# Performance work log

Hardware: AMD Instinct MI355X
Metric: run time of the kernel (lower is better)

The kernel has to match this reference:

```python
import jax, jax.numpy as jnp
import numpy as np

K = 10          # number of clusters (static; matches randint fill_max)
ALPHA = 0.02    # intra-cluster margin
DELTA = 0.5     # inter-cluster margin
LAMBDA_INTRA = 1.0
LAMBDA_INTER = 1.0
MIN_WEIGHT = 50.0


def setup_inputs() -> dict:
    key = jax.random.key(0)
    k1, k2 = jax.random.split(key)
    x = jax.random.normal(k1, (8, 64, 240, 320), dtype=jnp.float32)
    # module assumes NORMALIZED unit vectors along channel dim
    x = x / jnp.maximum(jnp.linalg.norm(x, axis=1, keepdims=True), 1e-12)
    cluster_masks = jax.random.randint(k2, (8, 1, 240, 320), 0, K, dtype=jnp.int32)
    return {"x": x, "cluster_masks": cluster_masks}


def reference(x, cluster_masks):
    B, C, H, W = x.shape
    cm = cluster_masks[:, 0]  # (B, H, W) int
    # one-hot cluster assignment; out-of-range ids (e.g. -1 = unlabeled) -> all zeros
    onehot = jax.nn.one_hot(cm, K, dtype=x.dtype)  # (B, H, W, K)

    # ---- spherical cluster means (fused segment-reduce over H*W) ----
    sums = jnp.einsum('bchw,bhwk->bck', x, onehot)          # (B, C, K)
    counts = jnp.sum(onehot, axis=(1, 2))                    # (B, K)
    means = sums / (counts[:, None, :] + 1e-10)
    # F.normalize(p=2, dim=1): x / max(||x||, eps)
    means = means / jnp.maximum(jnp.linalg.norm(means, axis=1, keepdims=True), 1e-12)

    # ---- broadcast means back to pixels ----
    tiled = jnp.einsum('bck,bhwk->bchw', means, onehot)      # (B, C, H, W)

    labeled = (cm >= 0).astype(x.dtype)                      # (B, H, W)
    # cosine metric
    intra_d = labeled * (0.5 * (1.0 - jnp.sum(x * tiled, axis=1)))  # (B, H, W)

    # ---- per-cluster hard-example weighting ----
    indicator = (intra_d > ALPHA).astype(x.dtype)            # (B, H, W)
    N_k = jnp.einsum('bhw,bhwk->bk', indicator, onehot)      # (B, K)
    weights = jnp.einsum('bk,bhwk->bhw', N_k, onehot)        # (B, H, W)
    weights = jnp.maximum(weights, MIN_WEIGHT) * K
    intra_loss = jnp.sum(intra_d ** 2 / weights) / B
    intra_loss = LAMBDA_INTRA * jnp.where(jnp.sum(indicator) > 0, intra_loss, 0.0)

    # ---- inter-cluster hinge loss (K > 1 statically) ----
    inter_d = 0.5 * (1.0 - jnp.einsum('bck,bcl->bkl', means, means))  # (B, K, K)
    hinge = jnp.maximum(DELTA - inter_d, 0.0) * (1.0 - jnp.eye(K, dtype=x.dtype))
    inter_loss = LAMBDA_INTER * jnp.sum(hinge ** 2) / (K * (K - 1) / 2 * B)

    loss = intra_loss + inter_loss
    return (loss, intra_loss, inter_loss)
```

## Files before the change

### kernel.cpp

```cpp
#include <hip/hip_runtime.h>

#define B_ 8
#define C_ 64
#define H_ 240
#define W_ 320
#define HW_ (H_ * W_)
#define HW4_ (HW_ / 4)
#define K_ 10
#define ALPHA_ 0.02f
#define DELTA_ 0.5f
#define MIN_WEIGHT_ 50.0f

#define NCH 4
#define CB_ (C_ / NCH)
#define Z1 8


__global__ __launch_bounds__(256) void k1_sums(
    const float* __restrict__ x, const int* __restrict__ cm,
    float* __restrict__ sums, float* __restrict__ counts) {
  const int cb = blockIdx.x;
  const int b = blockIdx.y;
  const int z = blockIdx.z;
  const int tid = threadIdx.x;
  const int c0 = cb * NCH;

  const int chunk = HW4_ / Z1;
  const int lo = z * chunk;
  const int hi = lo + chunk;

  const float4* __restrict__ xp =
      (const float4*)(x + (size_t)(b * C_ + c0) * HW_);
  const int4* __restrict__ cp = (const int4*)(cm + (size_t)b * HW_);

  float acc[NCH][K_];
#pragma unroll
  for (int c = 0; c < NCH; ++c)
#pragma unroll
    for (int j = 0; j < K_; ++j) acc[c][j] = 0.f;

  float cnt[K_];
#pragma unroll
  for (int j = 0; j < K_; ++j) cnt[j] = 0.f;
  const bool do_cnt = (cb == 0);

  for (int i = lo + tid; i < hi; i += 256) {
    const int4 k4 = cp[i];

    float oh0[K_], oh1[K_], oh2[K_], oh3[K_];
#pragma unroll
    for (int j = 0; j < K_; ++j) {
      oh0[j] = (k4.x == j) ? 1.f : 0.f;
      oh1[j] = (k4.y == j) ? 1.f : 0.f;
      oh2[j] = (k4.z == j) ? 1.f : 0.f;
      oh3[j] = (k4.w == j) ? 1.f : 0.f;
    }
    if (do_cnt) {
#pragma unroll
      for (int j = 0; j < K_; ++j)
        cnt[j] += (oh0[j] + oh1[j]) + (oh2[j] + oh3[j]);
    }

#pragma unroll
    for (int c = 0; c < NCH; ++c) {
      const float4 v = xp[c * HW4_ + i];
#pragma unroll
      for (int j = 0; j < K_; ++j) {
        acc[c][j] += v.x * oh0[j];
        acc[c][j] += v.y * oh1[j];
        acc[c][j] += v.z * oh2[j];
        acc[c][j] += v.w * oh3[j];
      }
    }
  }

#pragma unroll
  for (int c = 0; c < NCH; ++c) {
#pragma unroll
    for (int j = 0; j < K_; ++j) {
      float v = acc[c][j];
#pragma unroll
      for (int off = 32; off > 0; off >>= 1) v += __shfl_down(v, off, 64);
      if ((tid & 63) == 0)
        atomicAdd(&sums[(b * C_ + c0 + c) * K_ + j], v);
    }
  }
  if (do_cnt) {
#pragma unroll
    for (int j = 0; j < K_; ++j) {
      float v = cnt[j];
#pragma unroll
      for (int off = 32; off > 0; off >>= 1) v += __shfl_down(v, off, 64);
      if ((tid & 63) == 0) atomicAdd(&counts[b * K_ + j], v);
    }
  }
}

__global__ __launch_bounds__(256) void k3_intra(
    const float* __restrict__ x, const int* __restrict__ cm,
    const float* __restrict__ sums, const float* __restrict__ counts,
    float* __restrict__ means, float* __restrict__ S2,
    float* __restrict__ Nk) {
  const int b = blockIdx.y;
  const int chunk = blockIdx.x;
  const int tid = threadIdx.x;
  const int lane_p = tid & 63;
  const int grp = tid >> 6;

  __shared__ float mlds[C_ * K_];
  __shared__ float nrm[K_];
  __shared__ float4 pd[256];
  __shared__ float s2b[K_];
  __shared__ float nkb[K_];

  for (int i = tid; i < C_ * K_; i += 256) {
    const int k = i % K_;
    mlds[i] = sums[b * C_ * K_ + i] / (counts[b * K_ + k] + 1e-10f);
  }
  if (tid < K_) { s2b[tid] = 0.f; nkb[tid] = 0.f; }
  __syncthreads();
  if (tid < K_) {
    float n2 = 0.f;
#pragma unroll
    for (int c = 0; c < C_; ++c) {
      const float mm = mlds[c * K_ + tid];
      n2 += mm * mm;
    }
    nrm[tid] = 1.f / fmaxf(sqrtf(n2), 1e-12f);
  }
  __syncthreads();
  for (int i = tid; i < C_ * K_; i += 256) mlds[i] *= nrm[i % K_];
  __syncthreads();
  if (chunk == 0) {
    for (int i = tid; i < C_ * K_; i += 256) means[b * C_ * K_ + i] = mlds[i];
  }

  const int p4 = chunk * 64 + lane_p;
  const int4 k4 = ((const int4*)(cm + (size_t)b * HW_))[p4];
  const float4* __restrict__ xb = (const float4*)(x + (size_t)b * C_ * HW_);

  const int c0 = grp * (C_ / 4);
  const float* __restrict__ m0 = &mlds[c0 * K_ + k4.x];
  const float* __restrict__ m1 = &mlds[c0 * K_ + k4.y];
  const float* __restrict__ m2 = &mlds[c0 * K_ + k4.z];
  const float* __restrict__ m3 = &mlds[c0 * K_ + k4.w];

  float d0 = 0.f, d1 = 0.f, d2 = 0.f, d3 = 0.f;
#pragma unroll
  for (int cc = 0; cc < C_ / 4; ++cc) {
    const float4 v = xb[(c0 + cc) * HW4_ + p4];
    d0 += v.x * m0[cc * K_];
    d1 += v.y * m1[cc * K_];
    d2 += v.z * m2[cc * K_];
    d3 += v.w * m3[cc * K_];
  }
  pd[tid] = make_float4(d0, d1, d2, d3);
  __syncthreads();

  if (grp == 0) {
    float4 a = pd[lane_p];
    float4 bb = pd[lane_p + 64];
    float4 cc = pd[lane_p + 128];
    float4 dd = pd[lane_p + 192];
    const float i0 = 0.5f * (1.f - (a.x + bb.x + cc.x + dd.x));
    const float i1 = 0.5f * (1.f - (a.y + bb.y + cc.y + dd.y));
    const float i2 = 0.5f * (1.f - (a.z + bb.z + cc.z + dd.z));
    const float i3 = 0.5f * (1.f - (a.w + bb.w + cc.w + dd.w));

    atomicAdd(&s2b[k4.x], i0 * i0);
    atomicAdd(&s2b[k4.y], i1 * i1);
    atomicAdd(&s2b[k4.z], i2 * i2);
    atomicAdd(&s2b[k4.w], i3 * i3);
    atomicAdd(&nkb[k4.x], i0 > ALPHA_ ? 1.f : 0.f);
    atomicAdd(&nkb[k4.y], i1 > ALPHA_ ? 1.f : 0.f);
    atomicAdd(&nkb[k4.z], i2 > ALPHA_ ? 1.f : 0.f);
    atomicAdd(&nkb[k4.w], i3 > ALPHA_ ? 1.f : 0.f);
  }
  __syncthreads();

  if (tid < K_) {
    atomicAdd(&S2[b * K_ + tid], s2b[tid]);
    atomicAdd(&Nk[b * K_ + tid], nkb[tid]);
  }
}

__global__ __launch_bounds__(256) void k4_final(
    const float* __restrict__ means, const float* __restrict__ S2,
    const float* __restrict__ Nk, float* __restrict__ out) {
  const int tid = threadIdx.x;

  float acc_h = 0.f;
  for (int t = tid; t < B_ * 45; t += 256) {
    const int b = t / 45;
    int idx = t % 45;
    int k = 0, l = 0;
    for (k = 0; k < K_; ++k) {
      const int row = K_ - 1 - k;
      if (idx < row) { l = k + 1 + idx; break; }
      idx -= row;
    }
    float g = 0.f;
    for (int c = 0; c < C_; ++c)
      g += means[(b * C_ + c) * K_ + k] * means[(b * C_ + c) * K_ + l];
    const float inter_d = 0.5f * (1.f - g);
    const float h = fmaxf(DELTA_ - inter_d, 0.f);
    acc_h += 2.f * h * h;
  }

  float acc_i = 0.f;
  float acc_n = 0.f;
  if (tid < B_ * K_) {
    const float nk = Nk[tid];
    acc_n = nk;
    const float w = fmaxf(nk, MIN_WEIGHT_) * (float)K_;
    acc_i = S2[tid] / w;
  }

  __shared__ float rh[256], ri[256], rn[256];
  rh[tid] = acc_h;
  ri[tid] = acc_i;
  rn[tid] = acc_n;
  __syncthreads();
  for (int s = 128; s > 0; s >>= 1) {
    if (tid < s) {
      rh[tid] += rh[tid + s];
      ri[tid] += ri[tid + s];
      rn[tid] += rn[tid + s];
    }
    __syncthreads();
  }
  if (tid == 0) {
    const float inter = rh[0] / (float)((K_ * (K_ - 1) / 2) * B_);
    float intra = ri[0] / (float)B_;
    if (!(rn[0] > 0.f)) intra = 0.f;
    out[0] = intra + inter;
    out[1] = intra;
    out[2] = inter;
  }
}

extern "C" void kernel_launch(void* const* d_in, const int* in_sizes, int n_in,
                              void* d_out, int out_size, void* d_ws, size_t ws_size,
                              hipStream_t stream) {
  const float* x = (const float*)d_in[0];
  const int* cm = (const int*)d_in[1];

  float* ws = (float*)d_ws;
  float* sums = ws;
  float* counts = ws + 5120;
  float* S2 = ws + 5200;
  float* Nk = ws + 5280;
  float* means = ws + 5360;

  hipMemsetAsync(d_ws, 0, 5360 * sizeof(float), stream);

  k1_sums<<<dim3(CB_, B_, Z1), 256, 0, stream>>>(x, cm, sums, counts);
  k3_intra<<<dim3(HW4_ / 64, B_), 256, 0, stream>>>(x, cm, sums, counts, means,
                                                    S2, Nk);
  k4_final<<<1, 256, 0, stream>>>(means, S2, Nk, (float*)d_out);
}
```

Baseline: 285.9 us.

## Fuse three kernels into one persistent kernel with software grid barriers

Replaces the three separate launches (sums, intra distance, final reduction) with a single persistent kernel of 512 blocks that uses atomic-counter grid barriers between phases. Phase one splits pixels into 4 z-chunks instead of 8, and phase two loops over pixel chunks per block instead of one chunk per block. This removes kernel launch gaps and the tiny final-kernel launch, at the cost of spin-wait barriers that require all 512 blocks to be co-resident and fewer, longer-running blocks per phase.

```diff
diff --git a/kernel.cpp b/kernel.cpp
--- a/kernel.cpp
+++ b/kernel.cpp
@@ -11,231 +11,250 @@
 #define DELTA_ 0.5f
 #define MIN_WEIGHT_ 50.0f
 
+#define GRID_ 512
 #define NCH 4
-#define CB_ (C_ / NCH)
-#define Z1 8
-
-
-__global__ __launch_bounds__(256) void k1_sums(
+#define ZSPLIT 4
+#define CHUNK_A (HW4_ / ZSPLIT)
+
+
+__device__ __forceinline__ void grid_barrier(unsigned* cnt, unsigned* flag) {
+  __syncthreads();
+  if (threadIdx.x == 0) {
+    __threadfence();
+    if (atomicAdd(cnt, 1u) == GRID_ - 1u) {
+      __hip_atomic_store(flag, 1u, __ATOMIC_RELEASE, __HIP_MEMORY_SCOPE_AGENT);
+    } else {
+      while (__hip_atomic_load(flag, __ATOMIC_ACQUIRE,
+                               __HIP_MEMORY_SCOPE_AGENT) == 0u)
+        __builtin_amdgcn_s_sleep(8);
+    }
+  }
+  __syncthreads();
+  __threadfence();
+}
+
+__global__ __launch_bounds__(256, 2) void fused(
     const float* __restrict__ x, const int* __restrict__ cm,
-    float* __restrict__ sums, float* __restrict__ counts) {
-  const int cb = blockIdx.x;
-  const int b = blockIdx.y;
-  const int z = blockIdx.z;
+    float* __restrict__ ws, float* __restrict__ out) {
   const int tid = threadIdx.x;
-  const int c0 = cb * NCH;
-
-  const int chunk = HW4_ / Z1;
-  const int lo = z * chunk;
-  const int hi = lo + chunk;
-
-  const float4* __restrict__ xp =
-      (const float4*)(x + (size_t)(b * C_ + c0) * HW_);
-  const int4* __restrict__ cp = (const int4*)(cm + (size_t)b * HW_);
-
-  float acc[NCH][K_];
-#pragma unroll
-  for (int c = 0; c < NCH; ++c)
-#pragma unroll
-    for (int j = 0; j < K_; ++j) acc[c][j] = 0.f;
-
-  float cnt[K_];
-#pragma unroll
-  for (int j = 0; j < K_; ++j) cnt[j] = 0.f;
-  const bool do_cnt = (cb == 0);
-
-  for (int i = lo + tid; i < hi; i += 256) {
-    const int4 k4 = cp[i];
-
-    float oh0[K_], oh1[K_], oh2[K_], oh3[K_];
-#pragma unroll
-    for (int j = 0; j < K_; ++j) {
-      oh0[j] = (k4.x == j) ? 1.f : 0.f;
-      oh1[j] = (k4.y == j) ? 1.f : 0.f;
-      oh2[j] = (k4.z == j) ? 1.f : 0.f;
-      oh3[j] = (k4.w == j) ? 1.f : 0.f;
+  const int bid = blockIdx.x;
+
+  float* __restrict__ sums = ws;
+  float* __restrict__ counts = ws + 5120;
+  float* __restrict__ S2 = ws + 5200;
+  float* __restrict__ Nk = ws + 5280;
+  unsigned* bar = (unsigned*)(ws + 5360);
+  float* __restrict__ means = ws + 5376;
+
+  {
+    const int cb = bid & 15;
+    const int b = (bid >> 4) & 7;
+    const int z = bid >> 7;
+    const int c0 = cb * NCH;
+    const int lo = z * CHUNK_A;
+    const int hi = lo + CHUNK_A;
+
+    const float4* __restrict__ xp =
+        (const float4*)(x + (size_t)(b * C_ + c0) * HW_);
+    const int4* __restrict__ cp = (const int4*)(cm + (size_t)b * HW_);
+
+    float acc[NCH][K_];
+#pragma unroll
+    for (int c = 0; c < NCH; ++c)
+#pragma unroll
+      for (int j = 0; j < K_; ++j) acc[c][j] = 0.f;
+    float cnt[K_];
+#pragma unroll
+    for (int j = 0; j < K_; ++j) cnt[j] = 0.f;
+    const bool do_cnt = (cb == 0);
+
+    for (int i = lo + tid; i < hi; i += 256) {
+      const int4 k4 = cp[i];
+      float oh0[K_], oh1[K_], oh2[K_], oh3[K_];
+#pragma unroll
+      for (int j = 0; j < K_; ++j) {
+        oh0[j] = (k4.x == j) ? 1.f : 0.f;
+        oh1[j] = (k4.y == j) ? 1.f : 0.f;
+        oh2[j] = (k4.z == j) ? 1.f : 0.f;
+        oh3[j] = (k4.w == j) ? 1.f : 0.f;
+      }
+      if (do_cnt) {
+#pragma unroll
+        for (int j = 0; j < K_; ++j)
+          cnt[j] += (oh0[j] + oh1[j]) + (oh2[j] + oh3[j]);
+      }
+#pragma unroll
+      for (int c = 0; c < NCH; ++c) {
+        const float4 v = xp[c * HW4_ + i];
+#pragma unroll
+        for (int j = 0; j < K_; ++j) {
+          acc[c][j] += v.x * oh0[j];
+          acc[c][j] += v.y * oh1[j];
+          acc[c][j] += v.z * oh2[j];
+          acc[c][j] += v.w * oh3[j];
+        }
+      }
+    }
+
+#pragma unroll
+    for (int c = 0; c < NCH; ++c) {
+#pragma unroll
+      for (int j = 0; j < K_; ++j) {
+        float v = acc[c][j];
+#pragma unroll
+        for (int off = 32; off > 0; off >>= 1) v += __shfl_down(v, off, 64);
+        if ((tid & 63) == 0)
+          atomicAdd(&sums[(b * C_ + c0 + c) * K_ + j], v);
+      }
     }
     if (do_cnt) {
 #pragma unroll
-      for (int j = 0; j < K_; ++j)
-        cnt[j] += (oh0[j] + oh1[j]) + (oh2[j] + oh3[j]);
-    }
-
-#pragma unroll
-    for (int c = 0; c < NCH; ++c) {
-      const float4 v = xp[c * HW4_ + i];
-#pragma unroll
       for (int j = 0; j < K_; ++j) {
-        acc[c][j] += v.x * oh0[j];
-        acc[c][j] += v.y * oh1[j];
-        acc[c][j] += v.z * oh2[j];
-        acc[c][j] += v.w * oh3[j];
-      }
-    }
-  }
-
-#pragma unroll
-  for (int c = 0; c < NCH; ++c) {
-#pragma unroll
-    for (int j = 0; j < K_; ++j) {
-      float v = acc[c][j];
-#pragma unroll
-      for (int off = 32; off > 0; off >>= 1) v += __shfl_down(v, off, 64);
-      if ((tid & 63) == 0)
-        atomicAdd(&sums[(b * C_ + c0 + c) * K_ + j], v);
-    }
-  }
-  if (do_cnt) {
-#pragma unroll
-    for (int j = 0; j < K_; ++j) {
-      float v = cnt[j];
-#pragma unroll
-      for (int off = 32; off > 0; off >>= 1) v += __shfl_down(v, off, 64);
-      if ((tid & 63) == 0) atomicAdd(&counts[b * K_ + j], v);
-    }
-  }
-}
-
-__global__ __launch_bounds__(256) void k3_intra(
-    const float* __restrict__ x, const int* __restrict__ cm,
-    const float* __restrict__ sums, const float* __restrict__ counts,
-    float* __restrict__ means, float* __restrict__ S2,
-    float* __restrict__ Nk) {
-  const int b = blockIdx.y;
-  const int chunk = blockIdx.x;
-  const int tid = threadIdx.x;
-  const int lane_p = tid & 63;
-  const int grp = tid >> 6;
+        float v = cnt[j];
+#pragma unroll
+        for (int off = 32; off > 0; off >>= 1) v += __shfl_down(v, off, 64);
+        if ((tid & 63) == 0) atomicAdd(&counts[b * K_ + j], v);
+      }
+    }
+  }
+
+  grid_barrier(&bar[0], &bar[1]);
 
   __shared__ float mlds[C_ * K_];
   __shared__ float nrm[K_];
   __shared__ float4 pd[256];
   __shared__ float s2b[K_];
   __shared__ float nkb[K_];
-
-  for (int i = tid; i < C_ * K_; i += 256) {
-    const int k = i % K_;
-    mlds[i] = sums[b * C_ * K_ + i] / (counts[b * K_ + k] + 1e-10f);
-  }
-  if (tid < K_) { s2b[tid] = 0.f; nkb[tid] = 0.f; }
-  __syncthreads();
-  if (tid < K_) {
-    float n2 = 0.f;
-#pragma unroll
-    for (int c = 0; c < C_; ++c) {
-      const float mm = mlds[c * K_ + tid];
-      n2 += mm * mm;
-    }
-    nrm[tid] = 1.f / fmaxf(sqrtf(n2), 1e-12f);
-  }
-  __syncthreads();
-  for (int i = tid; i < C_ * K_; i += 256) mlds[i] *= nrm[i % K_];
-  __syncthreads();
-  if (chunk == 0) {
-    for (int i = tid; i < C_ * K_; i += 256) means[b * C_ * K_ + i] = mlds[i];
-  }
-
-  const int p4 = chunk * 64 + lane_p;
-  const int4 k4 = ((const int4*)(cm + (size_t)b * HW_))[p4];
-  const float4* __restrict__ xb = (const float4*)(x + (size_t)b * C_ * HW_);
-
-  const int c0 = grp * (C_ / 4);
-  const float* __restrict__ m0 = &mlds[c0 * K_ + k4.x];
-  const float* __restrict__ m1 = &mlds[c0 * K_ + k4.y];
-  const float* __restrict__ m2 = &mlds[c0 * K_ + k4.z];
-  const float* __restrict__ m3 = &mlds[c0 * K_ + k4.w];
-
-  float d0 = 0.f, d1 = 0.f, d2 = 0.f, d3 = 0.f;
-#pragma unroll
-  for (int cc = 0; cc < C_ / 4; ++cc) {
-    const float4 v = xb[(c0 + cc) * HW4_ + p4];
-    d0 += v.x * m0[cc * K_];
-    d1 += v.y * m1[cc * K_];
-    d2 += v.z * m2[cc * K_];
-    d3 += v.w * m3[cc * K_];
-  }
-  pd[tid] = make_float4(d0, d1, d2, d3);
-  __syncthreads();
-
-  if (grp == 0) {
-    float4 a = pd[lane_p];
-    float4 bb = pd[lane_p + 64];
-    float4 cc = pd[lane_p + 128];
-    float4 dd = pd[lane_p + 192];
-    const float i0 = 0.5f * (1.f - (a.x + bb.x + cc.x + dd.x));
-    const float i1 = 0.5f * (1.f - (a.y + bb.y + cc.y + dd.y));
-    const float i2 = 0.5f * (1.f - (a.z + bb.z + cc.z + dd.z));
-    const float i3 = 0.5f * (1.f - (a.w + bb.w + cc.w + dd.w));
-
-    atomicAdd(&s2b[k4.x], i0 * i0);
-    atomicAdd(&s2b[k4.y], i1 * i1);
-    atomicAdd(&s2b[k4.z], i2 * i2);
-    atomicAdd(&s2b[k4.w], i3 * i3);
-    atomicAdd(&nkb[k4.x], i0 > ALPHA_ ? 1.f : 0.f);
-    atomicAdd(&nkb[k4.y], i1 > ALPHA_ ? 1.f : 0.f);
-    atomicAdd(&nkb[k4.z], i2 > ALPHA_ ? 1.f : 0.f);
-    atomicAdd(&nkb[k4.w], i3 > ALPHA_ ? 1.f : 0.f);
-  }
-  __syncthreads();
-
-  if (tid < K_) {
-    atomicAdd(&S2[b * K_ + tid], s2b[tid]);
-    atomicAdd(&Nk[b * K_ + tid], nkb[tid]);
-  }
-}
-
-__global__ __launch_bounds__(256) void k4_final(
-    const float* __restrict__ means, const float* __restrict__ S2,
-    const float* __restrict__ Nk, float* __restrict__ out) {
-  const int tid = threadIdx.x;
-
-  float acc_h = 0.f;
-  for (int t = tid; t < B_ * 45; t += 256) {
-    const int b = t / 45;
-    int idx = t % 45;
-    int k = 0, l = 0;
-    for (k = 0; k < K_; ++k) {
-      const int row = K_ - 1 - k;
-      if (idx < row) { l = k + 1 + idx; break; }
-      idx -= row;
-    }
-    float g = 0.f;
-    for (int c = 0; c < C_; ++c)
-      g += means[(b * C_ + c) * K_ + k] * means[(b * C_ + c) * K_ + l];
-    const float inter_d = 0.5f * (1.f - g);
-    const float h = fmaxf(DELTA_ - inter_d, 0.f);
-    acc_h += 2.f * h * h;
-  }
-
-  float acc_i = 0.f;
-  float acc_n = 0.f;
-  if (tid < B_ * K_) {
-    const float nk = Nk[tid];
-    acc_n = nk;
-    const float w = fmaxf(nk, MIN_WEIGHT_) * (float)K_;
-    acc_i = S2[tid] / w;
-  }
-
-  __shared__ float rh[256], ri[256], rn[256];
-  rh[tid] = acc_h;
-  ri[tid] = acc_i;
-  rn[tid] = acc_n;
-  __syncthreads();
-  for (int s = 128; s > 0; s >>= 1) {
-    if (tid < s) {
-      rh[tid] += rh[tid + s];
-      ri[tid] += ri[tid + s];
-      rn[tid] += rn[tid + s];
-    }
-    __syncthreads();
-  }
-  if (tid == 0) {
-    const float inter = rh[0] / (float)((K_ * (K_ - 1) / 2) * B_);
-    float intra = ri[0] / (float)B_;
-    if (!(rn[0] > 0.f)) intra = 0.f;
-    out[0] = intra + inter;
-    out[1] = intra;
-    out[2] = inter;
+  {
+    const int b = bid >> 6;
+    const int cs = bid & 63;
+    const int lane_p = tid & 63;
+    const int grp = tid >> 6;
+
+    for (int i = tid; i < C_ * K_; i += 256) {
+      const int k = i % K_;
+      mlds[i] = sums[b * C_ * K_ + i] / (counts[b * K_ + k] + 1e-10f);
+    }
+    if (tid < K_) { s2b[tid] = 0.f; nkb[tid] = 0.f; }
+    __syncthreads();
+    if (tid < K_) {
+      float n2 = 0.f;
+#pragma unroll
+      for (int c = 0; c < C_; ++c) {
+        const float mm = mlds[c * K_ + tid];
+        n2 += mm * mm;
+      }
+      nrm[tid] = 1.f / fmaxf(sqrtf(n2), 1e-12f);
+    }
+    __syncthreads();
+    for (int i = tid; i < C_ * K_; i += 256) mlds[i] *= nrm[i % K_];
+    __syncthreads();
+    if (cs == 0) {
+      for (int i = tid; i < C_ * K_; i += 256) means[b * C_ * K_ + i] = mlds[i];
+    }
+
+    const float4* __restrict__ xb = (const float4*)(x + (size_t)b * C_ * HW_);
+    const int4* __restrict__ cmb = (const int4*)(cm + (size_t)b * HW_);
+    const int c0 = grp * (C_ / 4);
+
+    for (int chunk = cs; chunk < HW4_ / 64; chunk += 64) {
+      const int p4 = chunk * 64 + lane_p;
+      const int4 k4 = cmb[p4];
+      const float* __restrict__ m0 = &mlds[c0 * K_ + k4.x];
+      const float* __restrict__ m1 = &mlds[c0 * K_ + k4.y];
+      const float* __restrict__ m2 = &mlds[c0 * K_ + k4.z];
+      const float* __restrict__ m3 = &mlds[c0 * K_ + k4.w];
+
+      float d0 = 0.f, d1 = 0.f, d2 = 0.f, d3 = 0.f;
+#pragma unroll
+      for (int cc = 0; cc < C_ / 4; ++cc) {
+        const float4 v = xb[(c0 + cc) * HW4_ + p4];
+        d0 += v.x * m0[cc * K_];
+        d1 += v.y * m1[cc * K_];
+        d2 += v.z * m2[cc * K_];
+        d3 += v.w * m3[cc * K_];
+      }
+      pd[tid] = make_float4(d0, d1, d2, d3);
+      __syncthreads();
+
+      if (grp == 0) {
+        float4 a = pd[lane_p];
+        float4 bb = pd[lane_p + 64];
+        float4 cc = pd[lane_p + 128];
+        float4 dd = pd[lane_p + 192];
+        const float i0 = 0.5f * (1.f - (a.x + bb.x + cc.x + dd.x));
+        const float i1 = 0.5f * (1.f - (a.y + bb.y + cc.y + dd.y));
+        const float i2 = 0.5f * (1.f - (a.z + bb.z + cc.z + dd.z));
+        const float i3 = 0.5f * (1.f - (a.w + bb.w + cc.w + dd.w));
+
+        atomicAdd(&s2b[k4.x], i0 * i0);
+        atomicAdd(&s2b[k4.y], i1 * i1);
+        atomicAdd(&s2b[k4.z], i2 * i2);
+        atomicAdd(&s2b[k4.w], i3 * i3);
+        atomicAdd(&nkb[k4.x], i0 > ALPHA_ ? 1.f : 0.f);
+        atomicAdd(&nkb[k4.y], i1 > ALPHA_ ? 1.f : 0.f);
+        atomicAdd(&nkb[k4.z], i2 > ALPHA_ ? 1.f : 0.f);
+        atomicAdd(&nkb[k4.w], i3 > ALPHA_ ? 1.f : 0.f);
+      }
+      __syncthreads();
+    }
+
+    if (tid < K_) {
+      atomicAdd(&S2[b * K_ + tid], s2b[tid]);
+      atomicAdd(&Nk[b * K_ + tid], nkb[tid]);
+    }
+  }
+
+  grid_barrier(&bar[2], &bar[3]);
+
+  if (bid == 0) {
+    float acc_h = 0.f;
+    for (int t = tid; t < B_ * 45; t += 256) {
+      const int b = t / 45;
+      int idx = t % 45;
+      int k = 0, l = 0;
+      for (k = 0; k < K_; ++k) {
+        const int row = K_ - 1 - k;
+        if (idx < row) { l = k + 1 + idx; break; }
+        idx -= row;
+      }
+      float g = 0.f;
+      for (int c = 0; c < C_; ++c)
+        g += means[(b * C_ + c) * K_ + k] * means[(b * C_ + c) * K_ + l];
+      const float inter_d = 0.5f * (1.f - g);
+      const float h = fmaxf(DELTA_ - inter_d, 0.f);
+      acc_h += 2.f * h * h;
+    }
+
+    float acc_i = 0.f, acc_n = 0.f;
+    if (tid < B_ * K_) {
+      const float nk = Nk[tid];
+      acc_n = nk;
+      const float w = fmaxf(nk, MIN_WEIGHT_) * (float)K_;
+      acc_i = S2[tid] / w;
+    }
+
+    __shared__ float rh[256], ri[256], rn[256];
+    rh[tid] = acc_h;
+    ri[tid] = acc_i;
+    rn[tid] = acc_n;
+    __syncthreads();
+    for (int s = 128; s > 0; s >>= 1) {
+      if (tid < s) {
+        rh[tid] += rh[tid + s];
+        ri[tid] += ri[tid + s];
+        rn[tid] += rn[tid + s];
+      }
+      __syncthreads();
+    }
+    if (tid == 0) {
+      const float inter = rh[0] / (float)((K_ * (K_ - 1) / 2) * B_);
+      float intra = ri[0] / (float)B_;
+      if (!(rn[0] > 0.f)) intra = 0.f;
+      out[0] = intra + inter;
+      out[1] = intra;
+      out[2] = inter;
+    }
   }
 }
 
@@ -244,18 +263,9 @@
                               hipStream_t stream) {
   const float* x = (const float*)d_in[0];
   const int* cm = (const int*)d_in[1];
-
   float* ws = (float*)d_ws;
-  float* sums = ws;
-  float* counts = ws + 5120;
-  float* S2 = ws + 5200;
-  float* Nk = ws + 5280;
-  float* means = ws + 5360;
-
-  hipMemsetAsync(d_ws, 0, 5360 * sizeof(float), stream);
-
-  k1_sums<<<dim3(CB_, B_, Z1), 256, 0, stream>>>(x, cm, sums, counts);
-  k3_intra<<<dim3(HW4_ / 64, B_), 256, 0, stream>>>(x, cm, sums, counts, means,
-                                                    S2, Nk);
-  k4_final<<<1, 256, 0, stream>>>(means, S2, Nk, (float*)d_out);
+
+  hipMemsetAsync(d_ws, 0, 5376 * sizeof(float), stream);
+
+  fused<<<GRID_, 256, 0, stream>>>(x, cm, ws, (float*)d_out);
 }
```

Measured after the change: 444.7 us. 55.5% more time.

## Drop memset and final kernel via per-slice partials and last-block reduction

Applied to the files above, without the earlier changes.

k1 now writes per-z partial sums into distinct workspace slices through a shared-memory block reduction instead of global atomics, so the workspace memset is no longer needed. k3 sums those slices when it builds the means. The separate final kernel is folded into k3 using a completion counter, so only the last block computes the losses. This removes one memset and one kernel launch and their serialization gaps, at the cost of extra slice reads in every k3 block and reliance on k1 zeroing S2/Nk and the counter before k3 runs.

```diff
diff --git a/kernel.cpp b/kernel.cpp
--- a/kernel.cpp
+++ b/kernel.cpp
@@ -14,20 +14,28 @@
 #define NCH 4
 #define CB_ (C_ / NCH)
 #define Z1 8
-
+#define CHUNK1 (HW4_ / Z1)
+
+#define K3_BLOCKS (B_ * (HW4_ / 64))
+
+#define SL_SUMS 0
+#define SL_CNT  (Z1 * B_ * C_ * K_)
+#define OFF_S2  (SL_CNT + Z1 * B_ * K_)
+#define OFF_NK  (OFF_S2 + B_ * K_)
+#define OFF_DONE (OFF_NK + B_ * K_)
+#define OFF_MEANS 41792
 
 __global__ __launch_bounds__(256) void k1_sums(
     const float* __restrict__ x, const int* __restrict__ cm,
-    float* __restrict__ sums, float* __restrict__ counts) {
+    float* __restrict__ ws) {
   const int cb = blockIdx.x;
   const int b = blockIdx.y;
   const int z = blockIdx.z;
   const int tid = threadIdx.x;
   const int c0 = cb * NCH;
 
-  const int chunk = HW4_ / Z1;
-  const int lo = z * chunk;
-  const int hi = lo + chunk;
+  const int lo = z * CHUNK1;
+  const int hi = lo + CHUNK1;
 
   const float4* __restrict__ xp =
       (const float4*)(x + (size_t)(b * C_ + c0) * HW_);
@@ -38,7 +46,6 @@
   for (int c = 0; c < NCH; ++c)
 #pragma unroll
     for (int j = 0; j < K_; ++j) acc[c][j] = 0.f;
-
   float cnt[K_];
 #pragma unroll
   for (int j = 0; j < K_; ++j) cnt[j] = 0.f;
@@ -46,7 +53,6 @@
 
   for (int i = lo + tid; i < hi; i += 256) {
     const int4 k4 = cp[i];
-
     float oh0[K_], oh1[K_], oh2[K_], oh3[K_];
 #pragma unroll
     for (int j = 0; j < K_; ++j) {
@@ -60,7 +66,6 @@
       for (int j = 0; j < K_; ++j)
         cnt[j] += (oh0[j] + oh1[j]) + (oh2[j] + oh3[j]);
     }
-
 #pragma unroll
     for (int c = 0; c < NCH; ++c) {
       const float4 v = xp[c * HW4_ + i];
@@ -74,6 +79,9 @@
     }
   }
 
+  __shared__ float partS[4][NCH * K_];
+  __shared__ float partC[4][K_];
+  const int w = tid >> 6;
 #pragma unroll
   for (int c = 0; c < NCH; ++c) {
 #pragma unroll
@@ -81,8 +89,7 @@
       float v = acc[c][j];
 #pragma unroll
       for (int off = 32; off > 0; off >>= 1) v += __shfl_down(v, off, 64);
-      if ((tid & 63) == 0)
-        atomicAdd(&sums[(b * C_ + c0 + c) * K_ + j], v);
+      if ((tid & 63) == 0) partS[w][c * K_ + j] = v;
     }
   }
   if (do_cnt) {
@@ -91,33 +98,59 @@
       float v = cnt[j];
 #pragma unroll
       for (int off = 32; off > 0; off >>= 1) v += __shfl_down(v, off, 64);
-      if ((tid & 63) == 0) atomicAdd(&counts[b * K_ + j], v);
-    }
-  }
+      if ((tid & 63) == 0) partC[w][j] = v;
+    }
+  }
+  __syncthreads();
+
+  float* __restrict__ slice =
+      ws + SL_SUMS + z * (B_ * C_ * K_) + (b * C_ + c0) * K_;
+  for (int i = tid; i < NCH * K_; i += 256)
+    slice[i] = (partS[0][i] + partS[1][i]) + (partS[2][i] + partS[3][i]);
+  if (do_cnt && tid < K_) {
+    ws[SL_CNT + z * (B_ * K_) + b * K_ + tid] =
+        (partC[0][tid] + partC[1][tid]) + (partC[2][tid] + partC[3][tid]);
+  }
+
+  if (cb == 0 && b == 0 && z == 0 && tid < 161) ws[OFF_S2 + tid] = 0.f;
 }
 
 __global__ __launch_bounds__(256) void k3_intra(
     const float* __restrict__ x, const int* __restrict__ cm,
-    const float* __restrict__ sums, const float* __restrict__ counts,
-    float* __restrict__ means, float* __restrict__ S2,
-    float* __restrict__ Nk) {
+    float* __restrict__ ws, float* __restrict__ out) {
   const int b = blockIdx.y;
   const int chunk = blockIdx.x;
   const int tid = threadIdx.x;
   const int lane_p = tid & 63;
   const int grp = tid >> 6;
 
+  float* __restrict__ S2 = ws + OFF_S2;
+  float* __restrict__ Nk = ws + OFF_NK;
+  float* __restrict__ means = ws + OFF_MEANS;
+
+  __shared__ float cntl[K_];
   __shared__ float mlds[C_ * K_];
   __shared__ float nrm[K_];
   __shared__ float4 pd[256];
   __shared__ float s2b[K_];
   __shared__ float nkb[K_];
 
+  if (tid < K_) {
+    float s = 0.f;
+#pragma unroll
+    for (int z = 0; z < Z1; ++z) s += ws[SL_CNT + z * (B_ * K_) + b * K_ + tid];
+    cntl[tid] = s;
+    s2b[tid] = 0.f;
+    nkb[tid] = 0.f;
+  }
+  __syncthreads();
   for (int i = tid; i < C_ * K_; i += 256) {
-    const int k = i % K_;
-    mlds[i] = sums[b * C_ * K_ + i] / (counts[b * K_ + k] + 1e-10f);
-  }
-  if (tid < K_) { s2b[tid] = 0.f; nkb[tid] = 0.f; }
+    float s = 0.f;
+#pragma unroll
+    for (int z = 0; z < Z1; ++z)
+      s += ws[SL_SUMS + z * (B_ * C_ * K_) + b * C_ * K_ + i];
+    mlds[i] = s / (cntl[i % K_] + 1e-10f);
+  }
   __syncthreads();
   if (tid < K_) {
     float n2 = 0.f;
@@ -182,16 +215,23 @@
     atomicAdd(&S2[b * K_ + tid], s2b[tid]);
     atomicAdd(&Nk[b * K_ + tid], nkb[tid]);
   }
-}
-
-__global__ __launch_bounds__(256) void k4_final(
-    const float* __restrict__ means, const float* __restrict__ S2,
-    const float* __restrict__ Nk, float* __restrict__ out) {
-  const int tid = threadIdx.x;
+  __syncthreads();
+
+  __shared__ unsigned lastf;
+  if (tid == 0) {
+    __threadfence();
+    lastf = (atomicAdd((unsigned*)(ws + OFF_DONE), 1u) ==
+             (unsigned)(K3_BLOCKS - 1))
+                ? 1u
+                : 0u;
+  }
+  __syncthreads();
+  if (lastf == 0u) return;
+  __threadfence();
 
   float acc_h = 0.f;
   for (int t = tid; t < B_ * 45; t += 256) {
-    const int b = t / 45;
+    const int bb = t / 45;
     int idx = t % 45;
     int k = 0, l = 0;
     for (k = 0; k < K_; ++k) {
@@ -201,14 +241,13 @@
     }
     float g = 0.f;
     for (int c = 0; c < C_; ++c)
-      g += means[(b * C_ + c) * K_ + k] * means[(b * C_ + c) * K_ + l];
+      g += means[(bb * C_ + c) * K_ + k] * means[(bb * C_ + c) * K_ + l];
     const float inter_d = 0.5f * (1.f - g);
     const float h = fmaxf(DELTA_ - inter_d, 0.f);
     acc_h += 2.f * h * h;
   }
 
-  float acc_i = 0.f;
-  float acc_n = 0.f;
+  float acc_i = 0.f, acc_n = 0.f;
   if (tid < B_ * K_) {
     const float nk = Nk[tid];
     acc_n = nk;
@@ -244,18 +283,8 @@
                               hipStream_t stream) {
   const float* x = (const float*)d_in[0];
   const int* cm = (const int*)d_in[1];
-
   float* ws = (float*)d_ws;
-  float* sums = ws;
-  float* counts = ws + 5120;
-  float* S2 = ws + 5200;
-  float* Nk = ws + 5280;
-  float* means = ws + 5360;
-
-  hipMemsetAsync(d_ws, 0, 5360 * sizeof(float), stream);
-
-  k1_sums<<<dim3(CB_, B_, Z1), 256, 0, stream>>>(x, cm, sums, counts);
-  k3_intra<<<dim3(HW4_ / 64, B_), 256, 0, stream>>>(x, cm, sums, counts, means,
-                                                    S2, Nk);
-  k4_final<<<1, 256, 0, stream>>>(means, S2, Nk, (float*)d_out);
+
+  k1_sums<<<dim3(CB_, B_, Z1), 256, 0, stream>>>(x, cm, ws);
+  k3_intra<<<dim3(HW4_ / 64, B_), 256, 0, stream>>>(x, cm, ws, (float*)d_out);
 }
```

Result: slower. 341.0 us (+19.2%).
